# Performance work log

Measured on AMD Instinct MI355X. Metric: run time of the kernel, lower is better.

## Reference

```python
import jax, jax.numpy as jnp
import numpy as np

N_HEADS = 4
N_HIDDEN = 256  # out_features with concat=False
SLOPE = 0.1
NEG_INF = -9e15


def setup_inputs() -> dict:
    key = jax.random.key(0)
    k1, k2, k3, k4 = jax.random.split(key, 4)
    N, F_IN = 4096, 512
    h = jax.random.normal(k1, (N, F_IN), dtype=jnp.float32)
    adj_mat = jax.random.randint(k2, (N, N), 0, 2, dtype=jnp.int32)
    # xavier_normal gain=1.414
    W = jax.random.normal(k3, (F_IN, N_HIDDEN * N_HEADS), dtype=jnp.float32) * (
        1.414 * np.sqrt(2.0 / (F_IN + N_HIDDEN * N_HEADS)))
    a = jax.random.normal(k4, (N_HEADS, 2 * N_HIDDEN, 1), dtype=jnp.float32) * (
        1.414 * np.sqrt(2.0 / (2 * N_HIDDEN + 1)))
    return {"h": h, "adj_mat": adj_mat, "W": W, "a": a}


def reference(h, adj_mat, W, a):
    N = h.shape[0]
    # [N, H*D] -> [H, N, D]
    ht = (h @ W).reshape(N, N_HEADS, N_HIDDEN).transpose(1, 0, 2)
    lr = jax.nn.leaky_relu(ht, SLOPE)
    # additive attention: a split into source/target halves
    src = jnp.einsum('hnd,hd->hn', lr, a[:, :N_HIDDEN, 0])   # [H, N]
    tgt = jnp.einsum('hnd,hd->hn', lr, a[:, N_HIDDEN:, 0])   # [H, N]
    e = src[:, :, None] + tgt[:, None, :]                    # [H, N, N]
    e = jnp.where(adj_mat > 0, e, NEG_INF)
    attn = jax.nn.softmax(e, axis=-1)
    out = jnp.einsum('hnm,hmd->hnd', attn, ht)               # [H, N, D]
    return out.mean(axis=0)                                  # concat=False -> mean over heads
```

## Files before the change

### kernel.cpp

```cpp
#include <hip/hip_runtime.h>

#define N_NODES 4096
#define F_IN 512
#define NHID 256
#define HD 1024
#define NPAD 1152

typedef _Float16 half8 __attribute__((ext_vector_type(8)));
typedef _Float16 half4 __attribute__((ext_vector_type(4)));
typedef float floatx4 __attribute__((ext_vector_type(4)));
typedef float float4v __attribute__((ext_vector_type(4)));
typedef int int4v __attribute__((ext_vector_type(4)));
typedef unsigned int uint4v __attribute__((ext_vector_type(4)));

__device__ __forceinline__ float bf2f(unsigned short u) {
  union { unsigned int i; float f; } x; x.i = ((unsigned int)u) << 16; return x.f;
}

__device__ __forceinline__ void async_copy16(const void* g, void* l) {
  __builtin_amdgcn_global_load_lds((const __attribute__((address_space(1))) void*)g,
                                   (__attribute__((address_space(3))) void*)l, 16, 0, 0);
}

__global__ void detect_kernel(const unsigned short* __restrict__ hbits, int* __restrict__ flag) {
  const int t = threadIdx.x;
  int cnt = 0;
  for (int i = t; i < 1024; i += 256) {
    int e = (hbits[i] >> 7) & 0xFF;
    cnt += (e >= 115 && e <= 135) ? 1 : 0;
  }
  __shared__ int red[256];
  red[t] = cnt; __syncthreads();
  for (int s = 128; s > 0; s >>= 1) { if (t < s) red[t] += red[t + s]; __syncthreads(); }
  if (t == 0) flag[0] = (red[0] >= 900) ? 1 : 0;
}

template <typename OutT>
__device__ __forceinline__ void gemm_core(
    const _Float16* __restrict__ A, const _Float16* __restrict__ BT,
    OutT* __restrict__ C, int K, int ldc, int klen, long csz,
    int lin, int nbx, int nby, int total,
    _Float16* __restrict__ sA, _Float16* __restrict__ sB)
{
  int tile = ((total & 7) == 0) ? ((lin & 7) * (total >> 3) + (lin >> 3)) : lin;
  const int n_idx = tile % nbx;
  const int rem   = tile / nbx;
  const int m_idx = rem % nby;
  const int kz    = rem / nby;

  const int n0 = n_idx * 128;
  const int m0 = m_idx * 128;
  const int kbeg = kz * klen;
  OutT* Cz = C + (long)kz * csz;

  const int t = threadIdx.x;
  const int w = t >> 6;
  const int lane = t & 63;
  const int wm = (w >> 1) << 6;
  const int wn = (w & 1) << 6;

  floatx4 acc[4][4] = {};

  const int l4 = lane >> 2;
  const int kk = (lane & 3) << 3;
  const int c0 = w << 1;

  const _Float16* gA = A + (long)m0 * K;
  const _Float16* gBT = BT + (long)n0 * K;

  const int koff = (lane >> 4) << 3;
  const int rA = wm + (lane & 15);
  const int rB = wn + (lane & 15);

  const int nt = klen >> 5;

  auto STAGE = [&](int buf, int k0) {
#pragma unroll
    for (int p = 0; p < 2; ++p) {
      const int c = c0 + p;
      const int row = c * 16 + l4;
      async_copy16(gA + (long)row * K + k0 + kk, &sA[buf * 4096 + c * 512 + lane * 8]);
      async_copy16(gBT + (long)row * K + k0 + kk, &sB[buf * 4096 + c * 512 + lane * 8]);
    }
  };

  STAGE(0, kbeg);
  if (nt > 1) STAGE(1, kbeg + 32);

  int cur = 0;
  for (int it = 0; it < nt; ++it) {
    const int k0 = kbeg + it * 32;

    if (it + 1 < nt) asm volatile("s_waitcnt vmcnt(4)" ::: "memory");
    else             asm volatile("s_waitcnt vmcnt(0)" ::: "memory");
    __builtin_amdgcn_s_barrier();

    half8 af[4], bf[4];
#pragma unroll
    for (int i = 0; i < 4; ++i)
      af[i] = *(const half8*)&sA[cur * 4096 + (rA + i * 16) * 32 + koff];
#pragma unroll
    for (int i = 0; i < 4; ++i)
      bf[i] = *(const half8*)&sB[cur * 4096 + (rB + i * 16) * 32 + koff];

    asm volatile("s_waitcnt lgkmcnt(0)" ::: "memory");
    __builtin_amdgcn_sched_barrier(0);
    __builtin_amdgcn_s_barrier();

    const int nxt = (cur + 2 >= 3) ? cur - 1 : cur + 2;
    if (it + 2 < nt) STAGE(nxt, k0 + 64);

#pragma unroll
    for (int i = 0; i < 4; ++i)
#pragma unroll
      for (int j = 0; j < 4; ++j)
        acc[i][j] = __builtin_amdgcn_mfma_f32_16x16x32_f16(af[i], bf[j], acc[i][j], 0, 0, 0);

    cur = (cur + 1 >= 3) ? 0 : cur + 1;
  }

  const int q4 = (lane >> 4) << 2;
#pragma unroll
  for (int i = 0; i < 4; ++i) {
#pragma unroll
    for (int j = 0; j < 4; ++j) {
      const int gr = m0 + wm + i * 16 + q4;
      const int gc = n0 + wn + j * 16 + (lane & 15);
#pragma unroll
      for (int r = 0; r < 4; ++r)
        Cz[(long)(gr + r) * ldc + gc] = (OutT)acc[i][j][r];
    }
  }
}

template <typename OutT>
__global__ __launch_bounds__(256) void gemm_bt(
    const _Float16* __restrict__ A, const _Float16* __restrict__ BT,
    OutT* __restrict__ C, int K, int ldc, int klen, long csz)
{
  __shared__ _Float16 sA[3 * 128 * 32];
  __shared__ _Float16 sB[3 * 128 * 32];
  const int nbx = gridDim.x, nby = gridDim.y;
  const int total = nbx * nby * gridDim.z;
  const int lin = blockIdx.x + nbx * (blockIdx.y + nby * blockIdx.z);
  gemm_core<OutT>(A, BT, C, K, ldc, klen, csz, lin, nbx, nby, total, sA, sB);
}

__global__ __launch_bounds__(256) void fused_ht_cvt_kernel(
    const _Float16* __restrict__ hF, const _Float16* __restrict__ WT,
    _Float16* __restrict__ ht, const int* __restrict__ adj,
    _Float16* __restrict__ adjF)
{
  __shared__ _Float16 sA[3 * 128 * 32];
  __shared__ _Float16 sB[3 * 128 * 32];
  const int b = blockIdx.x;
  if (b < 256) {
    gemm_core<_Float16>(hF, WT, ht, F_IN, HD, F_IN, 0, b, 8, 32, 256, sA, sB);
  } else {
    const int i = (b - 256) * 256 + threadIdx.x;
    int4v A = ((const int4v*)adj)[2 * i];
    int4v B = ((const int4v*)adj)[2 * i + 1];
    half8 o;
#pragma unroll
    for (int e = 0; e < 4; ++e) {
      o[e]     = (_Float16)(A[e] > 0 ? 1.0f : 0.0f);
      o[4 + e] = (_Float16)(B[e] > 0 ? 1.0f : 0.0f);
    }
    ((half8*)adjF)[i] = o;
  }
}

__global__ void cvt_h_kernel(const void* __restrict__ in, _Float16* __restrict__ out,
                             const int* __restrict__ flag, int n8) {
  int i = blockIdx.x * 256 + threadIdx.x;
  if (i >= n8) return;
  half8 o;
  if (*flag) {
    union { uint4v v; unsigned short s[8]; } u;
    u.v = ((const uint4v*)in)[i];
#pragma unroll
    for (int e = 0; e < 8; ++e) o[e] = (_Float16)bf2f(u.s[e]);
  } else {
    const float4v* f = (const float4v*)in + 2 * i;
    float4v x0 = f[0], x1 = f[1];
#pragma unroll
    for (int e = 0; e < 4; ++e) { o[e] = (_Float16)x0[e]; o[4 + e] = (_Float16)x1[e]; }
  }
  ((half8*)out)[i] = o;
}

__global__ void cvt_a_kernel(const void* __restrict__ a, float* __restrict__ aF,
                             const int* __restrict__ flag) {
  const int t = threadIdx.x;
  const int bf = *flag;
#pragma unroll
  for (int e = 0; e < 8; ++e) {
    int idx = t * 8 + e;
    aF[idx] = bf ? bf2f(((const unsigned short*)a)[idx]) : ((const float*)a)[idx];
  }
}

__global__ void transpose_w_kernel(const void* __restrict__ W, _Float16* __restrict__ WT,
                                   const int* __restrict__ flag) {
  __shared__ _Float16 tile[64][72];
  const int k0 = blockIdx.x * 64, n0 = blockIdx.y * 64;
  const int t = threadIdx.x, r = t >> 3, c = t & 7;
  const int bf = *flag;
#pragma unroll
  for (int q = 0; q < 2; ++q) {
    int k = r + q * 32;
    half8 v;
    if (bf) {
      union { uint4v vv; unsigned short s[8]; } u;
      u.vv = *(const uint4v*)&((const unsigned short*)W)[(long)(k0 + k) * HD + n0 + c * 8];
#pragma unroll
      for (int e = 0; e < 8; ++e) v[e] = (_Float16)bf2f(u.s[e]);
    } else {
      const float4v* f = (const float4v*)&((const float*)W)[(long)(k0 + k) * HD + n0 + c * 8];
      float4v x0 = f[0], x1 = f[1];
#pragma unroll
      for (int e = 0; e < 4; ++e) { v[e] = (_Float16)x0[e]; v[4 + e] = (_Float16)x1[e]; }
    }
    *(half8*)&tile[k][c * 8] = v;
  }
  __syncthreads();
#pragma unroll
  for (int q = 0; q < 2; ++q) {
    int n = r + q * 32;
    half8 o;
#pragma unroll
    for (int e = 0; e < 8; ++e) o[e] = tile[c * 8 + e][n];
    *(half8*)&WT[(long)(n0 + n) * F_IN + k0 + c * 8] = o;
  }
}

__global__ void tgt_kernel(const _Float16* __restrict__ ht, const float* __restrict__ aF,
                           float* __restrict__ tgt) {
  const int i = blockIdx.x;
  const int t = threadIdx.x, h = t >> 6, lane = t & 63;
  half4 v = *(const half4*)&ht[(long)i * HD + h * NHID + lane * 4];
  float4v av = *(const float4v*)&aF[h * 512 + NHID + lane * 4];
  float s = 0.f;
#pragma unroll
  for (int e = 0; e < 4; ++e) {
    float x = (float)v[e];
    x = x > 0.f ? x : 0.1f * x;
    s += x * av[e];
  }
#pragma unroll
  for (int o = 32; o > 0; o >>= 1) s += __shfl_down(s, o);
  if (lane == 0) tgt[h * N_NODES + i] = s;
}

__global__ void maxexp_kernel(const float* __restrict__ tgt, float* __restrict__ wbuf,
                              _Float16* __restrict__ VT) {
  const int h = blockIdx.x, t = threadIdx.x;
  const float* row = tgt + h * N_NODES;
  float4v v[4];
  float m = -3.0e38f;
#pragma unroll
  for (int q = 0; q < 4; ++q) {
    v[q] = *(const float4v*)&row[(t + q * 256) * 4];
#pragma unroll
    for (int e = 0; e < 4; ++e) m = fmaxf(m, v[q][e]);
  }
#pragma unroll
  for (int o = 32; o > 0; o >>= 1) m = fmaxf(m, __shfl_down(m, o));
  __shared__ float red[4];
  if ((t & 63) == 0) red[t >> 6] = m;
  __syncthreads();
  m = fmaxf(fmaxf(red[0], red[1]), fmaxf(red[2], red[3]));
#pragma unroll
  for (int q = 0; q < 4; ++q) {
    const int j0 = (t + q * 256) * 4;
    float4v wv;
#pragma unroll
    for (int e = 0; e < 4; ++e) wv[e] = __expf(v[q][e] - m);
    *(float4v*)&wbuf[h * N_NODES + j0] = wv;
    half4 hv;
#pragma unroll
    for (int e = 0; e < 4; ++e) hv[e] = (_Float16)wv[e];
    *(half4*)&VT[(long)(HD + h) * N_NODES + j0] = hv;
  }
}

__global__ void scaled_transpose_kernel(const _Float16* __restrict__ ht, const float* __restrict__ wbuf,
                                        _Float16* __restrict__ VT) {
  __shared__ _Float16 tile[64][72];
  const int j0 = blockIdx.x * 64, n0 = blockIdx.y * 64;
  const int t = threadIdx.x, r = t >> 3, c = t & 7;
#pragma unroll
  for (int q = 0; q < 2; ++q) {
    int j = r + q * 32;
    *(half8*)&tile[j][c * 8] = *(const half8*)&ht[(long)(j0 + j) * HD + n0 + c * 8];
  }
  __syncthreads();
  const int h = n0 >> 8;
  const float* wrow = wbuf + h * N_NODES + j0;
#pragma unroll
  for (int q = 0; q < 2; ++q) {
    int n = r + q * 32;
    half8 o;
#pragma unroll
    for (int e = 0; e < 8; ++e) {
      int j = c * 8 + e;
      o[e] = (_Float16)(wrow[j] * (float)tile[j][n]);
    }
    *(half8*)&VT[(long)(n0 + n) * N_NODES + j0 + c * 8] = o;
  }
}

__global__ void epilogue_kernel(const float* __restrict__ S, float* __restrict__ out, int ns) {
  const int i = blockIdx.x, d = threadIdx.x;
  const long SZ = (long)N_NODES * NPAD;
  float num[4] = {0.f, 0.f, 0.f, 0.f};
  float den[4] = {0.f, 0.f, 0.f, 0.f};
  for (int z = 0; z < ns; ++z) {
    const float* row = S + z * SZ + (long)i * NPAD;
#pragma unroll
    for (int h = 0; h < 4; ++h) {
      num[h] += row[h * NHID + d];
      den[h] += row[HD + h];
    }
  }
  float r = 0.f;
#pragma unroll
  for (int h = 0; h < 4; ++h) r += num[h] / den[h];
  out[(long)i * NHID + d] = 0.25f * r;
}

extern "C" void kernel_launch(void* const* d_in, const int* in_sizes, int n_in,
                              void* d_out, int out_size, void* d_ws, size_t ws_size,
                              hipStream_t stream) {
  const void* h = nullptr; const int* adj = nullptr; const void* W = nullptr; const void* a = nullptr;
  for (int i = 0; i < n_in; ++i) {
    switch (in_sizes[i]) {
      case 2097152:  h   = d_in[i]; break;
      case 16777216: adj = (const int*)d_in[i]; break;
      case 524288:   W   = d_in[i]; break;
      case 2048:     a   = d_in[i]; break;
      default: break;
    }
  }
  float* out = (float*)d_out;

  char* ws = (char*)d_ws;
  const size_t OFF_ADJF = 0;
  const size_t OFF_VT   = 33554432;
  const size_t OFF_TGT  = OFF_VT + 9437184;
  const size_t OFF_WBUF = OFF_TGT + 65536;
  const size_t OFF_M    = OFF_WBUF + 65536;
  const size_t OFF_AF   = OFF_M + 256;
  const size_t OFF_X    = OFF_AF + 8192;
  const size_t SPART    = 18874368;

  int ns = 1;
  if      (ws_size >= OFF_X + 4 * SPART) ns = 4;
  else if (ws_size >= OFF_X + 2 * SPART) ns = 2;
  if (ws_size < OFF_X + SPART || !h || !adj || !W || !a) return;

  _Float16* adjF = (_Float16*)(ws + OFF_ADJF);
  _Float16* VT   = (_Float16*)(ws + OFF_VT);
  float*    tgt  = (float*)(ws + OFF_TGT);
  float*    wbuf = (float*)(ws + OFF_WBUF);
  int*      flag = (int*)(ws + OFF_M + 32);
  float*    aF   = (float*)(ws + OFF_AF);
  _Float16* hF = (_Float16*)(ws + OFF_X);
  _Float16* WT = (_Float16*)(ws + OFF_X + 4194304);
  _Float16* ht = (_Float16*)(ws + OFF_X + 5242880);
  float*    S  = (float*)(ws + OFF_X);

  detect_kernel<<<1, 256, 0, stream>>>((const unsigned short*)h, flag);
  cvt_h_kernel<<<1024, 256, 0, stream>>>(h, hF, flag, 262144);
  cvt_a_kernel<<<1, 256, 0, stream>>>(a, aF, flag);
  transpose_w_kernel<<<dim3(8, 16), 256, 0, stream>>>(W, WT, flag);
  fused_ht_cvt_kernel<<<8448, 256, 0, stream>>>(hF, WT, ht, adj, adjF);
  tgt_kernel<<<4096, 256, 0, stream>>>(ht, aF, tgt);
  maxexp_kernel<<<4, 256, 0, stream>>>(tgt, wbuf, VT);
  scaled_transpose_kernel<<<dim3(64, 16), 256, 0, stream>>>(ht, wbuf, VT);
  gemm_bt<float><<<dim3(9, 32, ns), 256, 0, stream>>>(adjF, VT, S, N_NODES, NPAD,
                                                      N_NODES / ns, (long)N_NODES * NPAD);
  epilogue_kernel<<<4096, 256, 0, stream>>>(S, out, ns);
}
```

Measured before the change: 200.3 us.

## Load int adjacency directly into GEMM registers, dropping fp16 adjacency conversion pass

The adjacency matrix is now read as int32 straight from global memory into registers inside the aggregation GEMM, clamped and packed to fp16 ones/zeros on the fly, so the separate pass that wrote a 32MB fp16 adjacency copy and re-read it is removed. The A operand bypasses LDS entirely and is prefetched in registers one k-step ahead, while only B is staged through LDS. The aggregation GEMM moves to 512-thread blocks with 256-row tiles, and the h@W GEMM uses the same register-A path in its own kernel. In exchange, the GEMM reads twice as many bytes for A (int32 instead of fp16) and uses more registers, with uncoalesced per-lane row loads.

```diff
diff --git a/kernel.cpp b/kernel.cpp
--- a/kernel.cpp
+++ b/kernel.cpp
@@ -35,13 +35,15 @@
   if (t == 0) flag[0] = (red[0] >= 900) ? 1 : 0;
 }
 
-template <typename OutT>
-__device__ __forceinline__ void gemm_core(
-    const _Float16* __restrict__ A, const _Float16* __restrict__ BT,
+template <int NT, bool AINT, typename OutT>
+__device__ __forceinline__ void gemm_areg(
+    const void* __restrict__ Av, const _Float16* __restrict__ BT,
     OutT* __restrict__ C, int K, int ldc, int klen, long csz,
-    int lin, int nbx, int nby, int total,
-    _Float16* __restrict__ sA, _Float16* __restrict__ sB)
+    int lin, int nbx, int nby, int total, _Float16* __restrict__ sB)
 {
+  constexpr int BM = NT / 2;
+  constexpr int LB = (NT == 512) ? 1 : 2;
+
   int tile = ((total & 7) == 0) ? ((lin & 7) * (total >> 3) + (lin >> 3)) : lin;
   const int n_idx = tile % nbx;
   const int rem   = tile / nbx;
@@ -49,7 +51,7 @@
   const int kz    = rem / nby;
 
   const int n0 = n_idx * 128;
-  const int m0 = m_idx * 128;
+  const int m0 = m_idx * BM;
   const int kbeg = kz * klen;
   OutT* Cz = C + (long)kz * csz;
 
@@ -61,62 +63,111 @@
 
   floatx4 acc[4][4] = {};
 
-  const int l4 = lane >> 2;
-  const int kk = (lane & 3) << 3;
-  const int c0 = w << 1;
-
-  const _Float16* gA = A + (long)m0 * K;
+  const int koff = (lane >> 4) << 3;
+  const int rB = wn + (lane & 15);
+  const int arow = m0 + wm + (lane & 15);
+
   const _Float16* gBT = BT + (long)n0 * K;
-
-  const int koff = (lane >> 4) << 3;
-  const int rA = wm + (lane & 15);
-  const int rB = wn + (lane & 15);
+  const int brow = t >> 2, bko = (t & 3) << 3;
+
+  auto STAGE_B = [&](int buf, int k0) {
+    async_copy16(gBT + (long)brow * K + k0 + bko, &sB[buf * 4096 + t * 8]);
+    if constexpr (NT == 256)
+      async_copy16(gBT + (long)(64 + brow) * K + k0 + bko, &sB[buf * 4096 + 2048 + t * 8]);
+  };
 
   const int nt = klen >> 5;
-
-  auto STAGE = [&](int buf, int k0) {
-#pragma unroll
-    for (int p = 0; p < 2; ++p) {
-      const int c = c0 + p;
-      const int row = c * 16 + l4;
-      async_copy16(gA + (long)row * K + k0 + kk, &sA[buf * 4096 + c * 512 + lane * 8]);
-      async_copy16(gBT + (long)row * K + k0 + kk, &sB[buf * 4096 + c * 512 + lane * 8]);
-    }
-  };
-
-  STAGE(0, kbeg);
-  if (nt > 1) STAGE(1, kbeg + 32);
-
+  int k0 = kbeg;
   int cur = 0;
-  for (int it = 0; it < nt; ++it) {
-    const int k0 = kbeg + it * 32;
-
-    if (it + 1 < nt) asm volatile("s_waitcnt vmcnt(4)" ::: "memory");
-    else             asm volatile("s_waitcnt vmcnt(0)" ::: "memory");
-    __builtin_amdgcn_s_barrier();
-
-    half8 af[4], bf[4];
-#pragma unroll
-    for (int i = 0; i < 4; ++i)
-      af[i] = *(const half8*)&sA[cur * 4096 + (rA + i * 16) * 32 + koff];
-#pragma unroll
-    for (int i = 0; i < 4; ++i)
-      bf[i] = *(const half8*)&sB[cur * 4096 + (rB + i * 16) * 32 + koff];
-
-    asm volatile("s_waitcnt lgkmcnt(0)" ::: "memory");
-    __builtin_amdgcn_sched_barrier(0);
-    __builtin_amdgcn_s_barrier();
-
-    const int nxt = (cur + 2 >= 3) ? cur - 1 : cur + 2;
-    if (it + 2 < nt) STAGE(nxt, k0 + 64);
-
-#pragma unroll
-    for (int i = 0; i < 4; ++i)
+
+  if constexpr (AINT) {
+    const int* Ai = (const int*)Av;
+    int4v ar[4][2];
+    auto LOAD_A = [&](int kk) {
+#pragma unroll
+      for (int i = 0; i < 4; ++i) {
+        const int* p = Ai + (long)(arow + i * 16) * K + kk + koff;
+        ar[i][0] = *(const int4v*)p;
+        ar[i][1] = *(const int4v*)(p + 4);
+      }
+    };
+    LOAD_A(k0);
+    STAGE_B(0, k0);
+    if (nt > 1) STAGE_B(1, k0 + 32);
+
+    for (int it = 0; it < nt; ++it) {
+      if (it + 1 < nt) asm volatile("s_waitcnt vmcnt(%0)" :: "i"(LB) : "memory");
+      else             asm volatile("s_waitcnt vmcnt(0)" ::: "memory");
+      __builtin_amdgcn_s_barrier();
+
+      half8 af[4];
+#pragma unroll
+      for (int i = 0; i < 4; ++i) {
+        union { unsigned int u[4]; half8 h; } pk;
+#pragma unroll
+        for (int e = 0; e < 4; ++e) {
+          const int4v& v = ar[i][e >> 1];
+          unsigned lo = (unsigned)v[(e & 1) << 1];
+          unsigned hi = (unsigned)v[((e & 1) << 1) + 1];
+          lo = lo < 1u ? lo : 1u;  hi = hi < 1u ? hi : 1u;
+          pk.u[e] = (lo + (hi << 16)) * 0x3C00u;
+        }
+        af[i] = pk.h;
+      }
+
+      half8 bf[4];
 #pragma unroll
       for (int j = 0; j < 4; ++j)
-        acc[i][j] = __builtin_amdgcn_mfma_f32_16x16x32_f16(af[i], bf[j], acc[i][j], 0, 0, 0);
-
-    cur = (cur + 1 >= 3) ? 0 : cur + 1;
+        bf[j] = *(const half8*)&sB[cur * 4096 + (rB + j * 16) * 32 + koff];
+
+      if (it + 1 < nt) LOAD_A(k0 + 32);
+      const int nxt = (cur + 2 >= 3) ? cur - 1 : cur + 2;
+      if (it + 2 < nt) STAGE_B(nxt, k0 + 64);
+
+      asm volatile("s_waitcnt lgkmcnt(0)" ::: "memory");
+      __builtin_amdgcn_sched_barrier(0);
+#pragma unroll
+      for (int i = 0; i < 4; ++i)
+#pragma unroll
+        for (int j = 0; j < 4; ++j)
+          acc[i][j] = __builtin_amdgcn_mfma_f32_16x16x32_f16(af[i], bf[j], acc[i][j], 0, 0, 0);
+      cur = (cur + 1 >= 3) ? 0 : cur + 1;
+      k0 += 32;
+    }
+  } else {
+    const _Float16* Af = (const _Float16*)Av;
+    half8 afP[4], afQ[4];
+    auto LOAD_AF = [&](half8 (&dst)[4], int kk) {
+#pragma unroll
+      for (int i = 0; i < 4; ++i)
+        dst[i] = *(const half8*)(Af + (long)(arow + i * 16) * K + kk + koff);
+    };
+    LOAD_AF(afP, k0);
+    STAGE_B(0, k0);
+    if (nt > 1) STAGE_B(1, k0 + 32);
+
+    auto BODY = [&](half8 (&use)[4], half8 (&fill)[4], int it) {
+      if (it + 1 < nt) asm volatile("s_waitcnt vmcnt(%0)" :: "i"(LB) : "memory");
+      else             asm volatile("s_waitcnt vmcnt(0)" ::: "memory");
+      __builtin_amdgcn_s_barrier();
+      half8 bf[4];
+#pragma unroll
+      for (int j = 0; j < 4; ++j)
+        bf[j] = *(const half8*)&sB[cur * 4096 + (rB + j * 16) * 32 + koff];
+      if (it + 1 < nt) LOAD_AF(fill, k0 + 32);
+      const int nxt = (cur + 2 >= 3) ? cur - 1 : cur + 2;
+      if (it + 2 < nt) STAGE_B(nxt, k0 + 64);
+      asm volatile("s_waitcnt lgkmcnt(0)" ::: "memory");
+      __builtin_amdgcn_sched_barrier(0);
+#pragma unroll
+      for (int i = 0; i < 4; ++i)
+#pragma unroll
+        for (int j = 0; j < 4; ++j)
+          acc[i][j] = __builtin_amdgcn_mfma_f32_16x16x32_f16(use[i], bf[j], acc[i][j], 0, 0, 0);
+      cur = (cur + 1 >= 3) ? 0 : cur + 1;
+      k0 += 32;
+    };
+    for (int it = 0; it < nt; it += 2) { BODY(afP, afQ, it); BODY(afQ, afP, it + 1); }
   }
 
   const int q4 = (lane >> 4) << 2;
@@ -133,41 +184,23 @@
   }
 }
 
-template <typename OutT>
-__global__ __launch_bounds__(256) void gemm_bt(
-    const _Float16* __restrict__ A, const _Float16* __restrict__ BT,
-    OutT* __restrict__ C, int K, int ldc, int klen, long csz)
+__global__ __launch_bounds__(512) void gemm_adj_kernel(
+    const int* __restrict__ adj, const _Float16* __restrict__ BT, float* __restrict__ C,
+    int K, int ldc, int klen, long csz)
 {
-  __shared__ _Float16 sA[3 * 128 * 32];
   __shared__ _Float16 sB[3 * 128 * 32];
   const int nbx = gridDim.x, nby = gridDim.y;
   const int total = nbx * nby * gridDim.z;
   const int lin = blockIdx.x + nbx * (blockIdx.y + nby * blockIdx.z);
-  gemm_core<OutT>(A, BT, C, K, ldc, klen, csz, lin, nbx, nby, total, sA, sB);
-}
-
-__global__ __launch_bounds__(256) void fused_ht_cvt_kernel(
-    const _Float16* __restrict__ hF, const _Float16* __restrict__ WT,
-    _Float16* __restrict__ ht, const int* __restrict__ adj,
-    _Float16* __restrict__ adjF)
+  gemm_areg<512, true, float>(adj, BT, C, K, ldc, klen, csz, lin, nbx, nby, total, sB);
+}
+
+__global__ __launch_bounds__(256) void gemm_ht_kernel(
+    const _Float16* __restrict__ hF, const _Float16* __restrict__ WT, _Float16* __restrict__ ht)
 {
-  __shared__ _Float16 sA[3 * 128 * 32];
   __shared__ _Float16 sB[3 * 128 * 32];
-  const int b = blockIdx.x;
-  if (b < 256) {
-    gemm_core<_Float16>(hF, WT, ht, F_IN, HD, F_IN, 0, b, 8, 32, 256, sA, sB);
-  } else {
-    const int i = (b - 256) * 256 + threadIdx.x;
-    int4v A = ((const int4v*)adj)[2 * i];
-    int4v B = ((const int4v*)adj)[2 * i + 1];
-    half8 o;
-#pragma unroll
-    for (int e = 0; e < 4; ++e) {
-      o[e]     = (_Float16)(A[e] > 0 ? 1.0f : 0.0f);
-      o[4 + e] = (_Float16)(B[e] > 0 ? 1.0f : 0.0f);
-    }
-    ((half8*)adjF)[i] = o;
-  }
+  const int lin = blockIdx.x + 8 * blockIdx.y;
+  gemm_areg<256, false, _Float16>(hF, WT, ht, F_IN, HD, F_IN, 0, lin, 8, 32, 256, sB);
 }
 
 __global__ void cvt_h_kernel(const void* __restrict__ in, _Float16* __restrict__ out,
@@ -345,8 +378,7 @@
   float* out = (float*)d_out;
 
   char* ws = (char*)d_ws;
-  const size_t OFF_ADJF = 0;
-  const size_t OFF_VT   = 33554432;
+  const size_t OFF_VT   = 0;
   const size_t OFF_TGT  = OFF_VT + 9437184;
   const size_t OFF_WBUF = OFF_TGT + 65536;
   const size_t OFF_M    = OFF_WBUF + 65536;
@@ -359,7 +391,6 @@
   else if (ws_size >= OFF_X + 2 * SPART) ns = 2;
   if (ws_size < OFF_X + SPART || !h || !adj || !W || !a) return;
 
-  _Float16* adjF = (_Float16*)(ws + OFF_ADJF);
   _Float16* VT   = (_Float16*)(ws + OFF_VT);
   float*    tgt  = (float*)(ws + OFF_TGT);
   float*    wbuf = (float*)(ws + OFF_WBUF);
@@ -374,11 +405,11 @@
   cvt_h_kernel<<<1024, 256, 0, stream>>>(h, hF, flag, 262144);
   cvt_a_kernel<<<1, 256, 0, stream>>>(a, aF, flag);
   transpose_w_kernel<<<dim3(8, 16), 256, 0, stream>>>(W, WT, flag);
-  fused_ht_cvt_kernel<<<8448, 256, 0, stream>>>(hF, WT, ht, adj, adjF);
+  gemm_ht_kernel<<<dim3(8, 32), 256, 0, stream>>>(hF, WT, ht);
   tgt_kernel<<<4096, 256, 0, stream>>>(ht, aF, tgt);
   maxexp_kernel<<<4, 256, 0, stream>>>(tgt, wbuf, VT);
   scaled_transpose_kernel<<<dim3(64, 16), 256, 0, stream>>>(ht, wbuf, VT);
-  gemm_bt<float><<<dim3(9, 32, ns), 256, 0, stream>>>(adjF, VT, S, N_NODES, NPAD,
-                                                      N_NODES / ns, (long)N_NODES * NPAD);
+  gemm_adj_kernel<<<dim3(9, 16, ns), 512, 0, stream>>>(adj, VT, S, N_NODES, NPAD,
+                                                       N_NODES / ns, (long)N_NODES * NPAD);
   epilogue_kernel<<<4096, 256, 0, stream>>>(S, out, ns);
 }
```

After: 375.5 us. 1.88x slower.
